# Kernel optimization log

Measured on AMD Instinct MI355X. Metric: run time of the kernel, lower is better.

## Reference

```python
import jax, jax.numpy as jnp
import numpy as np

KE_KCAL = 332.0636  # Coulomb constant, kcal/mol * Angstrom / e^2
R_CUT = 5.0
R_ON = R_CUT / 4.0
R_OFF = 3.0 * R_CUT / 4.0
B, A, F = 32, 1024, 128  # molecules, atoms per molecule, feature dim
MAX_Z = 86


def silu(x):
    return x * jax.nn.sigmoid(x)


def res_mlp(x, W1, W2, Wout):
    # Residual (two pre-activation linears) -> activation -> Linear, no biases
    h = silu(x) @ W1
    h = silu(h) @ W2
    return silu(x + h) @ Wout


def f_switch(r):
    # smooth switching function built from sigma(x)=exp(-1/x) for x>0 else 0
    arg = (r - R_ON) / (R_OFF - R_ON)
    def sigma(x):
        xs = jnp.where(x > 0, x, 1.0)
        return jnp.where(x > 0, jnp.exp(-1.0 / xs), 0.0)
    num = sigma(1.0 - arg)
    return num / (num + sigma(arg))


def setup_inputs() -> dict:
    key = jax.random.key(0)
    ks = jax.random.split(key, 16)
    box = 22.0  # ~liquid density box for 1024 atoms (Angstrom)
    s = 1.0 / np.sqrt(F)
    return {
        'e_z': jax.random.normal(ks[0], (B * A, F), jnp.float32) * 0.1,
        'charge': jax.random.normal(ks[1], (B,), jnp.float32),
        'xyz': jax.random.uniform(ks[2], (B, A, 3), jnp.float32) * box,
        'W_lin': jax.random.normal(ks[3], (F, F), jnp.float32) * s,
        'b_lin': jnp.zeros((F,), jnp.float32),
        'k_plus': jax.random.normal(ks[4], (F,), jnp.float32) * s,
        'k_minus': jax.random.normal(ks[5], (F,), jnp.float32) * s,
        'v_plus': jax.random.normal(ks[6], (F,), jnp.float32) * s,
        'v_minus': jax.random.normal(ks[7], (F,), jnp.float32) * s,
        'Wr1': jax.random.normal(ks[8], (F, F), jnp.float32) * s,
        'Wr2': jax.random.normal(ks[9], (F, F), jnp.float32) * s,
        'Wout': jax.random.normal(ks[10], (F, F), jnp.float32) * s,
        'w_e': jax.random.normal(ks[11], (F,), jnp.float32) * s,
        'q_z_table': jax.random.normal(ks[12], (MAX_Z,), jnp.float32) * 0.01,
        'z': jax.random.randint(ks[13], (B * A,), 1, MAX_Z, jnp.int32),
    }


def reference(e_z, charge, xyz, W_lin, b_lin, k_plus, k_minus, v_plus, v_minus,
              Wr1, Wr2, Wout, w_e, q_z_table, z):
    # ---- ElectronicEmbedding (per-molecule loop vectorized over B) ----
    q = (e_z @ W_lin + b_lin).reshape(B, A, F)
    pos = (charge >= 0)[:, None]                       # [B,1]
    k = jnp.where(pos, k_plus[None, :], k_minus[None, :])   # [B,F]
    v = jnp.where(pos, v_plus[None, :], v_minus[None, :])   # [B,F]
    arg = jnp.einsum('baf,bf->ba', q, k) / np.sqrt(F)
    num = jax.nn.softplus(arg)                         # log(1+exp)
    a = charge[:, None] * num / num.sum(axis=1, keepdims=True)  # [B,A]
    av = a[:, :, None] * v[:, None, :]                 # [B,A,F]
    e_psi = res_mlp(av.reshape(B * A, F), Wr1, Wr2, Wout)
    f = e_z + e_psi                                    # atom features [N,F]

    # ---- Electrostatics.get_charge (charge-conserving correction) ----
    pred_q = (f @ w_e + q_z_table[z]).reshape(B, A)
    corr = (charge - pred_q.sum(axis=1)) / A
    q_atom = pred_q + corr[:, None]                    # [B,A]

    # ---- Electrostatics.get_en: O(A^2) pairwise switched Coulomb ----
    diff = xyz[:, :, None, :] - xyz[:, None, :, :]     # [B,A,A,3]
    r2 = jnp.sum(diff * diff, axis=-1)                 # [B,A,A]
    mask = jnp.triu(jnp.ones((A, A), bool), k=1)       # pairs j > i (r>0)
    r = jnp.sqrt(jnp.where(mask, r2, 1.0))
    fs = f_switch(r)
    coul = fs / jnp.sqrt(r * r + 1.0) + (1.0 - fs) / r
    pair_e = q_atom[:, :, None] * q_atom[:, None, :] * coul
    energy = KE_KCAL * jnp.sum(jnp.where(mask, pair_e, 0.0), axis=(1, 2))  # [B]
    return energy
```

## Files before the change

### kernel.cpp

```cpp
#include <hip/hip_runtime.h>
#include <math.h>

#define B_MOL 32
#define A_AT  1024
#define NF    128
#define N_AT  (B_MOL * A_AT)

#define WS_K2P     0
#define WS_K2M     128
#define WS_WOUT    256
#define WS_C       384
#define WS_NUMSUM  512
#define WS_PREDSUM 544
#define WS_NUM     1024
#define WS_EZWE    (WS_NUM + N_AT)
#define WS_PRED    (WS_EZWE + N_AT)
#define WS_SIDX    (WS_PRED + N_AT)
#define WS_SPOS    (WS_SIDX + N_AT)
#define WS_W1F     (WS_SPOS + 4 * N_AT)
#define WS_W2F     (WS_W1F + 8192)

typedef short short8 __attribute__((ext_vector_type(8)));
typedef float floatx4 __attribute__((ext_vector_type(4)));

__device__ __forceinline__ float fast_rcp(float x) { return __builtin_amdgcn_rcpf(x); }
__device__ __forceinline__ float fast_rsq(float x) { return __builtin_amdgcn_rsqf(x); }
__device__ __forceinline__ float silu_f(float x) { return x * fast_rcp(1.f + __expf(-x)); }

__device__ __forceinline__ short f2bf(float x) {
  unsigned u = __float_as_uint(x);
  u += 0x7fffu + ((u >> 16) & 1u);
  return (short)(u >> 16);
}

__device__ __forceinline__ float wave_sum(float v) {
#pragma unroll
  for (int o = 32; o > 0; o >>= 1) v += __shfl_xor(v, o, 64);
  return v;
}

__global__ __launch_bounds__(256) void setup_kernel(const float* __restrict__ xyz,
                                                    const float* __restrict__ W_lin,
                                                    const float* __restrict__ b_lin,
                                                    const float* __restrict__ k_plus,
                                                    const float* __restrict__ k_minus,
                                                    const float* __restrict__ Wout,
                                                    const float* __restrict__ w_e,
                                                    const float* __restrict__ Wr1,
                                                    const float* __restrict__ Wr2,
                                                    float* __restrict__ ws,
                                                    float* __restrict__ out) {
  int bx = blockIdx.x, tid = threadIdx.x;
  if (bx < 32) {
    int mol = bx;
    __shared__ int hist[64], start[64];
    if (tid < 64) hist[tid] = 0;
    __syncthreads();
    float px[4], py[4], pz[4];
    int cell[4];
#pragma unroll
    for (int r = 0; r < 4; r++) {
      int j = tid + r * 256;
      const float* p = xyz + (size_t)(mol * A_AT + j) * 3;
      px[r] = p[0]; py[r] = p[1]; pz[r] = p[2];
      int cx = min(3, max(0, (int)(px[r] * (4.f / 22.f))));
      int cy = min(3, max(0, (int)(py[r] * (4.f / 22.f))));
      int cz = min(3, max(0, (int)(pz[r] * (4.f / 22.f))));
      cell[r] = cx * 16 + cy * 4 + cz;
      atomicAdd(&hist[cell[r]], 1);
    }
    __syncthreads();
    if (tid == 0) {
      int s = 0;
      for (int c = 0; c < 64; c++) { start[c] = s; s += hist[c]; }
    }
    __syncthreads();
    float4* spos = (float4*)(ws + WS_SPOS);
    int* sidx = (int*)ws + WS_SIDX;
#pragma unroll
    for (int r = 0; r < 4; r++) {
      int j = tid + r * 256;
      int off = atomicAdd(&start[cell[r]], 1);
      int g = mol * A_AT + off;
      spos[g] = make_float4(px[r], py[r], pz[r], 0.f);
      sidx[g] = j;
    }
  } else if (bx < 34) {
    const float* W = (bx == 32) ? Wr1 : Wr2;
    short* dst = (short*)(ws + ((bx == 32) ? WS_W1F : WS_W2F));
#pragma unroll
    for (int it = 0; it < 16; it++) {
      int idx = it * 256 + tid;
      int k = idx >> 5;
      int c0 = (idx & 31) * 4;
      float4 v = ((const float4*)W)[idx];
      int ks = k >> 5, q = (k & 31) >> 3, j = k & 7;
      float vv[4] = {v.x, v.y, v.z, v.w};
#pragma unroll
      for (int e = 0; e < 4; e++) {
        int col = c0 + e;
        int fi = (col >> 4) * 4 + ks;
        int lane = q * 16 + (col & 15);
        dst[fi * 512 + lane * 8 + j] = f2bf(vv[e]);
      }
    }
  } else {
    if (tid < 128) {
      float sp = 0.f, sm = 0.f;
      for (int f = 0; f < NF; f++) {
        float wl = W_lin[tid * NF + f];
        sp = fmaf(wl, k_plus[f], sp);
        sm = fmaf(wl, k_minus[f], sm);
      }
      ws[WS_K2P + tid] = sp;
      ws[WS_K2M + tid] = sm;
      if (tid < 2) {
        const float* kk = (tid == 0) ? k_plus : k_minus;
        float c = 0.f;
        for (int f = 0; f < NF; f++) c = fmaf(b_lin[f], kk[f], c);
        ws[WS_C + tid] = c;
      }
    } else {
      int g = tid - 128;
      float sw = 0.f;
      for (int f = 0; f < NF; f++) sw = fmaf(Wout[g * NF + f], w_e[f], sw);
      ws[WS_WOUT + g] = sw;
      if (g < 64) ws[WS_NUMSUM + g] = 0.f;
      if (g < 32) out[g] = 0.f;
    }
  }
}

__global__ __launch_bounds__(256) void attn_kernel(const float* __restrict__ e_z,
                                                   const float* __restrict__ charge,
                                                   const float* __restrict__ w_e,
                                                   float* __restrict__ ws) {
  int bx = blockIdx.x;
  int mol = bx >> 4;
  int base = bx * 64;
  int tid = threadIdx.x;
  int w = tid >> 6, l = tid & 63, half = l >> 5, l31 = l & 31;
  __shared__ float k2[NF], wesh[NF], numred[4];
  float ch = charge[mol];
  if (tid < 128) {
    const float* k2src = ws + (ch >= 0.f ? WS_K2P : WS_K2M);
    k2[tid] = k2src[tid];
    wesh[tid] = w_e[tid];
  }
  float cc = ws[WS_C + (ch >= 0.f ? 0 : 1)];
  __syncthreads();
  int b = l31 * 4;
  float k0 = k2[b], k1 = k2[b+1], k2v = k2[b+2], k3 = k2[b+3];
  float w0 = wesh[b], w1 = wesh[b+1], w2 = wesh[b+2], w3 = wesh[b+3];
  float wavenum = 0.f;
#pragma unroll
  for (int it = 0; it < 8; it++) {
    int m = it * 8 + w * 2 + half;
    int n = base + m;
    float4 v = *((const float4*)(e_z + (size_t)n * NF) + l31);
    float dk = v.x*k0; dk = fmaf(v.y, k1, dk); dk = fmaf(v.z, k2v, dk); dk = fmaf(v.w, k3, dk);
    float dw = v.x*w0; dw = fmaf(v.y, w1, dw); dw = fmaf(v.z, w2, dw); dw = fmaf(v.w, w3, dw);
#pragma unroll
    for (int o = 1; o < 32; o <<= 1) {
      dk += __shfl_xor(dk, o, 64);
      dw += __shfl_xor(dw, o, 64);
    }
    if (l31 == 0) {
      float arg = (dk + cc) * 0.08838834764831845f;
      float num = fmaxf(arg, 0.f) + log1pf(__expf(-fabsf(arg)));
      ws[WS_NUM + n] = num;
      ws[WS_EZWE + n] = dw;
      wavenum += num;
    }
  }
  wavenum += __shfl_xor(wavenum, 32, 64);
  if (l == 0) numred[w] = wavenum;
  __syncthreads();
  if (tid == 0)
    atomicAdd(&ws[WS_NUMSUM + mol], numred[0] + numred[1] + numred[2] + numred[3]);
}

__global__ __launch_bounds__(256) void mlp_kernel(const float* __restrict__ charge,
                                                  const float* __restrict__ v_plus,
                                                  const float* __restrict__ v_minus,
                                                  const int* __restrict__ z,
                                                  const float* __restrict__ qz_table,
                                                  float* __restrict__ ws) {
  int base = blockIdx.x * 64;
  int mol = base >> 10;
  int tid = threadIdx.x;
  int w = tid >> 6;
  int lane = tid & 63;
  int q = lane >> 4, l15 = lane & 15;

  __shared__ short wf[16384];
  __shared__ short a2s[4 * 16 * 136];
  __shared__ float vsh[NF], wout_sh[NF], awsh[64], pred_sh[64];

  float ch = charge[mol];
  if (tid < 128) {
    vsh[tid] = (ch >= 0.f) ? v_plus[tid] : v_minus[tid];
    wout_sh[tid] = ws[WS_WOUT + tid];
  }
  if (tid < 64) awsh[tid] = ch * ws[WS_NUM + base + tid] / ws[WS_NUMSUM + mol];

  {
    const float4* src = (const float4*)(ws + WS_W1F);
    float4* dst = (float4*)wf;
#pragma unroll
    for (int r = 0; r < 8; r++) dst[tid + r * 256] = src[tid + r * 256];
  }
  __syncthreads();

  float aw_m = awsh[w * 16 + l15];
  floatx4 acc1[8];
#pragma unroll
  for (int nt = 0; nt < 8; nt++) acc1[nt] = (floatx4)(0.f);

#pragma unroll
  for (int ks = 0; ks < 4; ks++) {
    float4 va = *(const float4*)&vsh[ks * 32 + q * 8];
    float4 vb = *(const float4*)&vsh[ks * 32 + q * 8 + 4];
    short8 af;
    af[0] = f2bf(silu_f(aw_m * va.x)); af[1] = f2bf(silu_f(aw_m * va.y));
    af[2] = f2bf(silu_f(aw_m * va.z)); af[3] = f2bf(silu_f(aw_m * va.w));
    af[4] = f2bf(silu_f(aw_m * vb.x)); af[5] = f2bf(silu_f(aw_m * vb.y));
    af[6] = f2bf(silu_f(aw_m * vb.z)); af[7] = f2bf(silu_f(aw_m * vb.w));
#pragma unroll
    for (int nt = 0; nt < 8; nt++) {
      short8 bf = *(const short8*)&wf[(nt * 4 + ks) * 512 + lane * 8];
      acc1[nt] = __builtin_amdgcn_mfma_f32_16x16x32_bf16(af, bf, acc1[nt], 0, 0, 0);
    }
  }

#pragma unroll
  for (int nt = 0; nt < 8; nt++) {
    int f = nt * 16 + l15;
#pragma unroll
    for (int r = 0; r < 4; r++)
      a2s[w * 2176 + (q * 4 + r) * 136 + f] = f2bf(silu_f(acc1[nt][r]));
  }
  __syncthreads();
  {
    const float4* src = (const float4*)(ws + WS_W2F);
    float4* dst = (float4*)wf;
#pragma unroll
    for (int r = 0; r < 8; r++) dst[tid + r * 256] = src[tid + r * 256];
  }
  __syncthreads();

  floatx4 acc2[8];
#pragma unroll
  for (int nt = 0; nt < 8; nt++) acc2[nt] = (floatx4)(0.f);

#pragma unroll
  for (int ks = 0; ks < 4; ks++) {
    short8 af = *(const short8*)&a2s[w * 2176 + l15 * 136 + ks * 32 + q * 8];
#pragma unroll
    for (int nt = 0; nt < 8; nt++) {
      short8 bf = *(const short8*)&wf[(nt * 4 + ks) * 512 + lane * 8];
      acc2[nt] = __builtin_amdgcn_mfma_f32_16x16x32_bf16(af, bf, acc2[nt], 0, 0, 0);
    }
  }

  float awq[4], part[4];
#pragma unroll
  for (int r = 0; r < 4; r++) {
    awq[r] = awsh[w * 16 + q * 4 + r];
    part[r] = 0.f;
  }
#pragma unroll
  for (int nt = 0; nt < 8; nt++) {
    int f = nt * 16 + l15;
    float vv = vsh[f], ww = wout_sh[f];
#pragma unroll
    for (int r = 0; r < 4; r++) {
      float s = silu_f(fmaf(awq[r], vv, acc2[nt][r]));
      part[r] = fmaf(s, ww, part[r]);
    }
  }
#pragma unroll
  for (int r = 0; r < 4; r++) {
#pragma unroll
    for (int o = 1; o < 16; o <<= 1) part[r] += __shfl_xor(part[r], o, 64);
  }
  if (l15 == 0) {
#pragma unroll
    for (int r = 0; r < 4; r++) {
      int m = w * 16 + q * 4 + r;
      int n = base + m;
      float pred = part[r] + ws[WS_EZWE + n] + qz_table[z[n]];
      ws[WS_PRED + n] = pred;
      pred_sh[m] = pred;
    }
  }
  __syncthreads();
  if (tid < 64) {
    float s = wave_sum(pred_sh[tid]);
    if (tid == 0) atomicAdd(&ws[WS_PREDSUM + mol], s);
  }
}

__global__ __launch_bounds__(256) void pair_kernel(const float* __restrict__ charge,
                                                   float* __restrict__ ws,
                                                   float* __restrict__ out) {
  int bx = blockIdx.x;
  int mol = bx >> 4;
  int s = bx & 15;
  int tid = threadIdx.x;
  int w = tid >> 6, lane = tid & 63;
  __shared__ float4 posq[1024];
  __shared__ float wred[4];
  const float4* spos = (const float4*)(ws + WS_SPOS);
  const int* sidx = (const int*)ws + WS_SIDX;
  float corr = (charge[mol] - ws[WS_PREDSUM + mol]) * (1.f / 1024.f);
  for (int j = tid; j < 1024; j += 256) {
    float4 p = spos[mol * 1024 + j];
    p.w = ws[WS_PRED + mol * 1024 + sidx[mol * 1024 + j]] + corr;
    posq[j] = p;
  }
  __syncthreads();
  int i = s * 64 + lane;
  float4 me = posq[i];
  float e = 0.f;
  for (int c = s + w; c < 16; c += 4) {
    int j0 = c * 64;
    if (c == s) {
#pragma unroll 4
      for (int j = j0; j < j0 + 64; j++) {
        float4 p = posq[j];
        float dx = me.x - p.x, dy = me.y - p.y, dz = me.z - p.z;
        float r2 = fmaf(dx, dx, fmaf(dy, dy, dz * dz));
        bool skip = (j <= i);
        float r2s = skip ? 1.0e8f : r2;
        float qj = skip ? 0.f : p.w;
        float inv_r = fast_rsq(r2s);
        e = fmaf(qj, inv_r, e);
        if (__any(r2s < 14.0625f)) {
          float r = r2s * inv_r;
          float arg = (r - 1.25f) * 0.4f;
          float argc = fminf(fmaxf(arg, 1e-6f), 1.f - 1e-6f);
          float t = fast_rcp(argc) - fast_rcp(1.f - argc);
          float fs = fast_rcp(1.f + __expf(-t));
          float delta = fs * (fast_rsq(r2s + 1.f) - inv_r);
          e = fmaf(qj, delta, e);
        }
      }
    } else {
#pragma unroll 4
      for (int j = j0; j < j0 + 64; j++) {
        float4 p = posq[j];
        float dx = me.x - p.x, dy = me.y - p.y, dz = me.z - p.z;
        float r2 = fmaf(dx, dx, fmaf(dy, dy, dz * dz));
        float qj = p.w;
        float inv_r = fast_rsq(r2);
        e = fmaf(qj, inv_r, e);
        if (__any(r2 < 14.0625f)) {
          float r = r2 * inv_r;
          float arg = (r - 1.25f) * 0.4f;
          float argc = fminf(fmaxf(arg, 1e-6f), 1.f - 1e-6f);
          float t = fast_rcp(argc) - fast_rcp(1.f - argc);
          float fs = fast_rcp(1.f + __expf(-t));
          float delta = fs * (fast_rsq(r2 + 1.f) - inv_r);
          e = fmaf(qj, delta, e);
        }
      }
    }
  }
  e *= me.w;
  float sred = wave_sum(e);
  if (lane == 0) wred[w] = sred;
  __syncthreads();
  if (tid == 0)
    atomicAdd(&out[mol], 332.0636f * (wred[0] + wred[1] + wred[2] + wred[3]));
}

extern "C" void kernel_launch(void* const* d_in, const int* in_sizes, int n_in,
                              void* d_out, int out_size, void* d_ws, size_t ws_size,
                              hipStream_t stream) {
  const float* e_z     = (const float*)d_in[0];
  const float* charge  = (const float*)d_in[1];
  const float* xyz     = (const float*)d_in[2];
  const float* W_lin   = (const float*)d_in[3];
  const float* b_lin   = (const float*)d_in[4];
  const float* k_plus  = (const float*)d_in[5];
  const float* k_minus = (const float*)d_in[6];
  const float* v_plus  = (const float*)d_in[7];
  const float* v_minus = (const float*)d_in[8];
  const float* Wr1     = (const float*)d_in[9];
  const float* Wr2     = (const float*)d_in[10];
  const float* Wout    = (const float*)d_in[11];
  const float* w_e     = (const float*)d_in[12];
  const float* qz      = (const float*)d_in[13];
  const int*   z       = (const int*)d_in[14];
  float* out = (float*)d_out;
  float* ws  = (float*)d_ws;

  setup_kernel<<<35, 256, 0, stream>>>(xyz, W_lin, b_lin, k_plus, k_minus,
                                       Wout, w_e, Wr1, Wr2, ws, out);
  attn_kernel<<<512, 256, 0, stream>>>(e_z, charge, w_e, ws);
  mlp_kernel<<<512, 256, 0, stream>>>(charge, v_plus, v_minus, z, qz, ws);
  pair_kernel<<<512, 256, 0, stream>>>(charge, ws, out);
}
```

Measured before the change: 147.9 us.

## Fuse setup, attention, MLP and pair kernels into one with per-molecule barriers

Replaces four separate kernel launches with one fused kernel of 512 blocks. Blocks of the same molecule synchronise through spin-wait atomic counters in global memory, which are reset by a memset. Per-block partial sums replace global atomics, and intermediates such as num and ezwe now stay in shared memory. Each block redundantly recomputes the small W_lin·k and Wout·w_e products, and the weight-fragment conversion moves into the blocks with s==1. This removes launch gaps and global round trips, but the spin barriers assume all 16 blocks of a molecule are co-resident, which risks deadlock if they are not.

```diff
diff --git a/kernel.cpp b/kernel.cpp
--- a/kernel.cpp
+++ b/kernel.cpp
@@ -6,19 +6,15 @@
 #define NF    128
 #define N_AT  (B_MOL * A_AT)
 
-#define WS_K2P     0
-#define WS_K2M     128
-#define WS_WOUT    256
-#define WS_C       384
-#define WS_NUMSUM  512
-#define WS_PREDSUM 544
-#define WS_NUM     1024
-#define WS_EZWE    (WS_NUM + N_AT)
-#define WS_PRED    (WS_EZWE + N_AT)
-#define WS_SIDX    (WS_PRED + N_AT)
-#define WS_SPOS    (WS_SIDX + N_AT)
-#define WS_W1F     (WS_SPOS + 4 * N_AT)
-#define WS_W2F     (WS_W1F + 8192)
+#define WS_FRAG1    0
+#define WS_FRAG2    8192
+#define WS_PRED     16384
+#define WS_SIDX     49152
+#define WS_SPOS     81920
+#define WS_NUMPART  212992
+#define WS_PREDPART 213504
+#define WS_ENERPART 214016
+#define WS_CTR      214528
 
 typedef short short8 __attribute__((ext_vector_type(8)));
 typedef float floatx4 __attribute__((ext_vector_type(4)));
@@ -39,21 +35,104 @@
   return v;
 }
 
-__global__ __launch_bounds__(256) void setup_kernel(const float* __restrict__ xyz,
-                                                    const float* __restrict__ W_lin,
-                                                    const float* __restrict__ b_lin,
-                                                    const float* __restrict__ k_plus,
-                                                    const float* __restrict__ k_minus,
-                                                    const float* __restrict__ Wout,
-                                                    const float* __restrict__ w_e,
-                                                    const float* __restrict__ Wr1,
-                                                    const float* __restrict__ Wr2,
-                                                    float* __restrict__ ws,
-                                                    float* __restrict__ out) {
+__device__ __forceinline__ void mol_barrier(unsigned* c) {
+  __threadfence();
+  __syncthreads();
+  if (threadIdx.x == 0) {
+    unsigned prev = __hip_atomic_fetch_add(c, 1u, __ATOMIC_ACQ_REL, __HIP_MEMORY_SCOPE_AGENT);
+    if (prev + 1u < 16u) {
+      while (__hip_atomic_load(c, __ATOMIC_ACQUIRE, __HIP_MEMORY_SCOPE_AGENT) < 16u)
+        __builtin_amdgcn_s_sleep(2);
+    }
+  }
+  __syncthreads();
+}
+
+__global__ __launch_bounds__(256, 2) void fused_kernel(
+    const float* __restrict__ e_z, const float* __restrict__ charge,
+    const float* __restrict__ xyz, const float* __restrict__ W_lin,
+    const float* __restrict__ b_lin, const float* __restrict__ k_plus,
+    const float* __restrict__ k_minus, const float* __restrict__ v_plus,
+    const float* __restrict__ v_minus, const float* __restrict__ Wr1,
+    const float* __restrict__ Wr2, const float* __restrict__ Wout,
+    const float* __restrict__ w_e, const float* __restrict__ qz_table,
+    const int* __restrict__ z, float* __restrict__ ws, float* __restrict__ out) {
   int bx = blockIdx.x, tid = threadIdx.x;
-  if (bx < 32) {
-    int mol = bx;
-    __shared__ int hist[64], start[64];
+  int mol = bx >> 4, s = bx & 15;
+  int base = bx * 64;
+
+  __shared__ __align__(16) char big[50176];
+  __shared__ float num_sh[64], ezwe_sh[64], wout_sh[128], awsh[64], vsh[128];
+  __shared__ float cc_sh, bsum_sh;
+
+  float* k2 = (float*)big;
+  float* wesh = k2 + 128;
+  int* hist = (int*)(wesh + 128);
+  int* startc = hist + 64;
+  float* numred = (float*)(startc + 64);
+  unsigned* ctr = (unsigned*)(ws + WS_CTR);
+
+  float ch = charge[mol];
+  bool cpos = ch >= 0.f;
+  const float* kvec = cpos ? k_plus : k_minus;
+
+  {
+    int r = tid & 127;
+    const float* M = (tid < 128) ? W_lin : Wout;
+    const float* vv = (tid < 128) ? kvec : w_e;
+    const float4* row = (const float4*)(M + (size_t)r * NF);
+    float acc = 0.f;
+#pragma unroll 8
+    for (int i = 0; i < 32; i++) {
+      float4 a = row[i];
+      float4 b = ((const float4*)vv)[i];
+      acc = fmaf(a.x, b.x, acc); acc = fmaf(a.y, b.y, acc);
+      acc = fmaf(a.z, b.z, acc); acc = fmaf(a.w, b.w, acc);
+    }
+    if (tid < 128) { k2[r] = acc; wesh[r] = w_e[r]; }
+    else wout_sh[r] = acc;
+  }
+  if (tid < 64) {
+    float c = b_lin[tid] * kvec[tid] + b_lin[tid + 64] * kvec[tid + 64];
+    c = wave_sum(c);
+    if (tid == 0) cc_sh = c;
+  }
+  __syncthreads();
+
+  int w = tid >> 6, l = tid & 63, half = l >> 5, l31 = l & 31;
+  {
+    int b4 = l31 * 4;
+    float ka = k2[b4], kb = k2[b4 + 1], kc = k2[b4 + 2], kd = k2[b4 + 3];
+    float wa = wesh[b4], wb = wesh[b4 + 1], wc = wesh[b4 + 2], wd = wesh[b4 + 3];
+    float cc = cc_sh;
+    float wavenum = 0.f;
+#pragma unroll
+    for (int it = 0; it < 8; it++) {
+      int m = it * 8 + w * 2 + half;
+      int n = base + m;
+      float4 v = *((const float4*)(e_z + (size_t)n * NF) + l31);
+      float dk = v.x * ka; dk = fmaf(v.y, kb, dk); dk = fmaf(v.z, kc, dk); dk = fmaf(v.w, kd, dk);
+      float dw = v.x * wa; dw = fmaf(v.y, wb, dw); dw = fmaf(v.z, wc, dw); dw = fmaf(v.w, wd, dw);
+#pragma unroll
+      for (int o = 1; o < 32; o <<= 1) {
+        dk += __shfl_xor(dk, o, 64);
+        dw += __shfl_xor(dw, o, 64);
+      }
+      if (l31 == 0) {
+        float arg = (dk + cc) * 0.08838834764831845f;
+        float num = fmaxf(arg, 0.f) + log1pf(__expf(-fabsf(arg)));
+        num_sh[m] = num;
+        ezwe_sh[m] = dw;
+        wavenum += num;
+      }
+    }
+    wavenum += __shfl_xor(wavenum, 32, 64);
+    if (l == 0) numred[w] = wavenum;
+  }
+  __syncthreads();
+  if (tid == 0) ws[WS_NUMPART + bx] = numred[0] + numred[1] + numred[2] + numred[3];
+
+  if (s == 0) {
     if (tid < 64) hist[tid] = 0;
     __syncthreads();
     float px[4], py[4], pz[4];
@@ -71,147 +150,66 @@
     }
     __syncthreads();
     if (tid == 0) {
-      int s = 0;
-      for (int c = 0; c < 64; c++) { start[c] = s; s += hist[c]; }
+      int acc = 0;
+      for (int c = 0; c < 64; c++) { startc[c] = acc; acc += hist[c]; }
     }
     __syncthreads();
     float4* spos = (float4*)(ws + WS_SPOS);
-    int* sidx = (int*)ws + WS_SIDX;
+    int* sidx = (int*)(ws + WS_SIDX);
 #pragma unroll
     for (int r = 0; r < 4; r++) {
       int j = tid + r * 256;
-      int off = atomicAdd(&start[cell[r]], 1);
+      int off = atomicAdd(&startc[cell[r]], 1);
       int g = mol * A_AT + off;
       spos[g] = make_float4(px[r], py[r], pz[r], 0.f);
       sidx[g] = j;
     }
-  } else if (bx < 34) {
-    const float* W = (bx == 32) ? Wr1 : Wr2;
-    short* dst = (short*)(ws + ((bx == 32) ? WS_W1F : WS_W2F));
-#pragma unroll
-    for (int it = 0; it < 16; it++) {
-      int idx = it * 256 + tid;
-      int k = idx >> 5;
-      int c0 = (idx & 31) * 4;
-      float4 v = ((const float4*)W)[idx];
-      int ks = k >> 5, q = (k & 31) >> 3, j = k & 7;
-      float vv[4] = {v.x, v.y, v.z, v.w};
-#pragma unroll
-      for (int e = 0; e < 4; e++) {
-        int col = c0 + e;
-        int fi = (col >> 4) * 4 + ks;
-        int lane = q * 16 + (col & 15);
-        dst[fi * 512 + lane * 8 + j] = f2bf(vv[e]);
+  }
+
+  if (s == 1) {
+#pragma unroll
+    for (int mtx = 0; mtx < 2; mtx++) {
+      const float* W = mtx ? Wr2 : Wr1;
+      short* dst = (short*)(ws + (mtx ? WS_FRAG2 : WS_FRAG1));
+#pragma unroll
+      for (int p = 0; p < 8; p++) {
+        int idx = p * 256 + tid;
+        int fi = idx >> 6, ln = idx & 63;
+        int nt = fi >> 2, ks = fi & 3;
+        int qq = ln >> 4, n15 = ln & 15;
+        int k0r = ks * 32 + qq * 8;
+        int col = nt * 16 + n15;
+        short8 v;
+#pragma unroll
+        for (int j = 0; j < 8; j++) v[j] = f2bf(W[(size_t)(k0r + j) * NF + col]);
+        *(short8*)(dst + (size_t)idx * 8) = v;
       }
     }
-  } else {
-    if (tid < 128) {
-      float sp = 0.f, sm = 0.f;
-      for (int f = 0; f < NF; f++) {
-        float wl = W_lin[tid * NF + f];
-        sp = fmaf(wl, k_plus[f], sp);
-        sm = fmaf(wl, k_minus[f], sm);
-      }
-      ws[WS_K2P + tid] = sp;
-      ws[WS_K2M + tid] = sm;
-      if (tid < 2) {
-        const float* kk = (tid == 0) ? k_plus : k_minus;
-        float c = 0.f;
-        for (int f = 0; f < NF; f++) c = fmaf(b_lin[f], kk[f], c);
-        ws[WS_C + tid] = c;
-      }
-    } else {
-      int g = tid - 128;
-      float sw = 0.f;
-      for (int f = 0; f < NF; f++) sw = fmaf(Wout[g * NF + f], w_e[f], sw);
-      ws[WS_WOUT + g] = sw;
-      if (g < 64) ws[WS_NUMSUM + g] = 0.f;
-      if (g < 32) out[g] = 0.f;
-    }
-  }
-}
-
-__global__ __launch_bounds__(256) void attn_kernel(const float* __restrict__ e_z,
-                                                   const float* __restrict__ charge,
-                                                   const float* __restrict__ w_e,
-                                                   float* __restrict__ ws) {
-  int bx = blockIdx.x;
-  int mol = bx >> 4;
-  int base = bx * 64;
-  int tid = threadIdx.x;
-  int w = tid >> 6, l = tid & 63, half = l >> 5, l31 = l & 31;
-  __shared__ float k2[NF], wesh[NF], numred[4];
-  float ch = charge[mol];
-  if (tid < 128) {
-    const float* k2src = ws + (ch >= 0.f ? WS_K2P : WS_K2M);
-    k2[tid] = k2src[tid];
-    wesh[tid] = w_e[tid];
-  }
-  float cc = ws[WS_C + (ch >= 0.f ? 0 : 1)];
-  __syncthreads();
-  int b = l31 * 4;
-  float k0 = k2[b], k1 = k2[b+1], k2v = k2[b+2], k3 = k2[b+3];
-  float w0 = wesh[b], w1 = wesh[b+1], w2 = wesh[b+2], w3 = wesh[b+3];
-  float wavenum = 0.f;
-#pragma unroll
-  for (int it = 0; it < 8; it++) {
-    int m = it * 8 + w * 2 + half;
-    int n = base + m;
-    float4 v = *((const float4*)(e_z + (size_t)n * NF) + l31);
-    float dk = v.x*k0; dk = fmaf(v.y, k1, dk); dk = fmaf(v.z, k2v, dk); dk = fmaf(v.w, k3, dk);
-    float dw = v.x*w0; dw = fmaf(v.y, w1, dw); dw = fmaf(v.z, w2, dw); dw = fmaf(v.w, w3, dw);
-#pragma unroll
-    for (int o = 1; o < 32; o <<= 1) {
-      dk += __shfl_xor(dk, o, 64);
-      dw += __shfl_xor(dw, o, 64);
-    }
-    if (l31 == 0) {
-      float arg = (dk + cc) * 0.08838834764831845f;
-      float num = fmaxf(arg, 0.f) + log1pf(__expf(-fabsf(arg)));
-      ws[WS_NUM + n] = num;
-      ws[WS_EZWE + n] = dw;
-      wavenum += num;
-    }
-  }
-  wavenum += __shfl_xor(wavenum, 32, 64);
-  if (l == 0) numred[w] = wavenum;
-  __syncthreads();
-  if (tid == 0)
-    atomicAdd(&ws[WS_NUMSUM + mol], numred[0] + numred[1] + numred[2] + numred[3]);
-}
-
-__global__ __launch_bounds__(256) void mlp_kernel(const float* __restrict__ charge,
-                                                  const float* __restrict__ v_plus,
-                                                  const float* __restrict__ v_minus,
-                                                  const int* __restrict__ z,
-                                                  const float* __restrict__ qz_table,
-                                                  float* __restrict__ ws) {
-  int base = blockIdx.x * 64;
-  int mol = base >> 10;
-  int tid = threadIdx.x;
-  int w = tid >> 6;
-  int lane = tid & 63;
-  int q = lane >> 4, l15 = lane & 15;
-
-  __shared__ short wf[16384];
-  __shared__ short a2s[4 * 16 * 136];
-  __shared__ float vsh[NF], wout_sh[NF], awsh[64], pred_sh[64];
-
-  float ch = charge[mol];
-  if (tid < 128) {
-    vsh[tid] = (ch >= 0.f) ? v_plus[tid] : v_minus[tid];
-    wout_sh[tid] = ws[WS_WOUT + tid];
-  }
-  if (tid < 64) awsh[tid] = ch * ws[WS_NUM + base + tid] / ws[WS_NUMSUM + mol];
-
+  }
+
+  mol_barrier(&ctr[mol]);
+
+  if (tid == 0) {
+    float t = 0.f;
+#pragma unroll
+    for (int i = 0; i < 16; i++) t += ws[WS_NUMPART + mol * 16 + i];
+    bsum_sh = t;
+  }
+  if (tid < 128) vsh[tid] = cpos ? v_plus[tid] : v_minus[tid];
+  __syncthreads();
+  if (tid < 64) awsh[tid] = ch * num_sh[tid] / bsum_sh;
+
+  short* wf = (short*)big;
+  short* a2s = (short*)(big + 32768);
   {
-    const float4* src = (const float4*)(ws + WS_W1F);
+    const float4* src = (const float4*)(ws + WS_FRAG1);
     float4* dst = (float4*)wf;
 #pragma unroll
     for (int r = 0; r < 8; r++) dst[tid + r * 256] = src[tid + r * 256];
   }
   __syncthreads();
 
+  int q = l >> 4, l15 = l & 15;
   float aw_m = awsh[w * 16 + l15];
   floatx4 acc1[8];
 #pragma unroll
@@ -228,7 +226,7 @@
     af[6] = f2bf(silu_f(aw_m * vb.z)); af[7] = f2bf(silu_f(aw_m * vb.w));
 #pragma unroll
     for (int nt = 0; nt < 8; nt++) {
-      short8 bf = *(const short8*)&wf[(nt * 4 + ks) * 512 + lane * 8];
+      short8 bf = *(const short8*)&wf[(nt * 4 + ks) * 512 + l * 8 + w * 0];
       acc1[nt] = __builtin_amdgcn_mfma_f32_16x16x32_bf16(af, bf, acc1[nt], 0, 0, 0);
     }
   }
@@ -242,7 +240,7 @@
   }
   __syncthreads();
   {
-    const float4* src = (const float4*)(ws + WS_W2F);
+    const float4* src = (const float4*)(ws + WS_FRAG2);
     float4* dst = (float4*)wf;
 #pragma unroll
     for (int r = 0; r < 8; r++) dst[tid + r * 256] = src[tid + r * 256];
@@ -258,7 +256,7 @@
     short8 af = *(const short8*)&a2s[w * 2176 + l15 * 136 + ks * 32 + q * 8];
 #pragma unroll
     for (int nt = 0; nt < 8; nt++) {
-      short8 bf = *(const short8*)&wf[(nt * 4 + ks) * 512 + lane * 8];
+      short8 bf = *(const short8*)&wf[(nt * 4 + ks) * 512 + l * 8];
       acc2[nt] = __builtin_amdgcn_mfma_f32_16x16x32_bf16(af, bf, acc2[nt], 0, 0, 0);
     }
   }
@@ -272,11 +270,11 @@
 #pragma unroll
   for (int nt = 0; nt < 8; nt++) {
     int f = nt * 16 + l15;
-    float vv = vsh[f], ww = wout_sh[f];
+    float vv = vsh[f], ww2 = wout_sh[f];
 #pragma unroll
     for (int r = 0; r < 4; r++) {
-      float s = silu_f(fmaf(awq[r], vv, acc2[nt][r]));
-      part[r] = fmaf(s, ww, part[r]);
+      float sfl = silu_f(fmaf(awq[r], vv, acc2[nt][r]));
+      part[r] = fmaf(sfl, ww2, part[r]);
     }
   }
 #pragma unroll
@@ -284,43 +282,44 @@
 #pragma unroll
     for (int o = 1; o < 16; o <<= 1) part[r] += __shfl_xor(part[r], o, 64);
   }
+  float* pred_shf = (float*)(big + 32768);
+  __syncthreads();
   if (l15 == 0) {
 #pragma unroll
     for (int r = 0; r < 4; r++) {
       int m = w * 16 + q * 4 + r;
       int n = base + m;
-      float pred = part[r] + ws[WS_EZWE + n] + qz_table[z[n]];
+      float pred = part[r] + ezwe_sh[m] + qz_table[z[n]];
       ws[WS_PRED + n] = pred;
-      pred_sh[m] = pred;
+      pred_shf[m] = pred;
     }
   }
   __syncthreads();
   if (tid < 64) {
-    float s = wave_sum(pred_sh[tid]);
-    if (tid == 0) atomicAdd(&ws[WS_PREDSUM + mol], s);
-  }
-}
-
-__global__ __launch_bounds__(256) void pair_kernel(const float* __restrict__ charge,
-                                                   float* __restrict__ ws,
-                                                   float* __restrict__ out) {
-  int bx = blockIdx.x;
-  int mol = bx >> 4;
-  int s = bx & 15;
-  int tid = threadIdx.x;
-  int w = tid >> 6, lane = tid & 63;
-  __shared__ float4 posq[1024];
-  __shared__ float wred[4];
+    float ssum = wave_sum(pred_shf[tid]);
+    if (tid == 0) ws[WS_PREDPART + bx] = ssum;
+  }
+
+  mol_barrier(&ctr[32 + mol]);
+
+  if (tid == 0) {
+    float t = 0.f;
+#pragma unroll
+    for (int i = 0; i < 16; i++) t += ws[WS_PREDPART + mol * 16 + i];
+    bsum_sh = t;
+  }
+  __syncthreads();
+  float corr = (ch - bsum_sh) * (1.f / 1024.f);
+  float4* posq = (float4*)big;
   const float4* spos = (const float4*)(ws + WS_SPOS);
-  const int* sidx = (const int*)ws + WS_SIDX;
-  float corr = (charge[mol] - ws[WS_PREDSUM + mol]) * (1.f / 1024.f);
+  const int* sidx = (const int*)(ws + WS_SIDX);
   for (int j = tid; j < 1024; j += 256) {
     float4 p = spos[mol * 1024 + j];
     p.w = ws[WS_PRED + mol * 1024 + sidx[mol * 1024 + j]] + corr;
     posq[j] = p;
   }
   __syncthreads();
-  int i = s * 64 + lane;
+  int i = s * 64 + l;
   float4 me = posq[i];
   float e = 0.f;
   for (int c = s + w; c < 16; c += 4) {
@@ -369,10 +368,20 @@
   }
   e *= me.w;
   float sred = wave_sum(e);
-  if (lane == 0) wred[w] = sred;
-  __syncthreads();
-  if (tid == 0)
-    atomicAdd(&out[mol], 332.0636f * (wred[0] + wred[1] + wred[2] + wred[3]));
+  if (l == 0) awsh[w] = sred;
+  __syncthreads();
+  if (tid == 0) {
+    ws[WS_ENERPART + bx] = 332.0636f * (awsh[0] + awsh[1] + awsh[2] + awsh[3]);
+    __threadfence();
+    unsigned prev = __hip_atomic_fetch_add(&ctr[64 + mol], 1u,
+                                           __ATOMIC_ACQ_REL, __HIP_MEMORY_SCOPE_AGENT);
+    if (prev == 15u) {
+      float tot = 0.f;
+#pragma unroll
+      for (int i2 = 0; i2 < 16; i2++) tot += ws[WS_ENERPART + mol * 16 + i2];
+      out[mol] = tot;
+    }
+  }
 }
 
 extern "C" void kernel_launch(void* const* d_in, const int* in_sizes, int n_in,
@@ -396,9 +405,8 @@
   float* out = (float*)d_out;
   float* ws  = (float*)d_ws;
 
-  setup_kernel<<<35, 256, 0, stream>>>(xyz, W_lin, b_lin, k_plus, k_minus,
-                                       Wout, w_e, Wr1, Wr2, ws, out);
-  attn_kernel<<<512, 256, 0, stream>>>(e_z, charge, w_e, ws);
-  mlp_kernel<<<512, 256, 0, stream>>>(charge, v_plus, v_minus, z, qz, ws);
-  pair_kernel<<<512, 256, 0, stream>>>(charge, ws, out);
+  hipMemsetAsync(ws + WS_CTR, 0, 96 * sizeof(unsigned), stream);
+  fused_kernel<<<512, 256, 0, stream>>>(e_z, charge, xyz, W_lin, b_lin,
+                                        k_plus, k_minus, v_plus, v_minus,
+                                        Wr1, Wr2, Wout, w_e, qz, z, ws, out);
 }
```

Measured after the change: 327.2 us. 121% more time.
